# Performance work log

Hardware: AMD Instinct MI355X
Metric: run time of the kernel (lower is better)

The kernel has to match this reference:

```python
import jax, jax.numpy as jnp
import numpy as np

N = 100000
E = 1600000
IN_DIM = 64
H_DIM = 64
OUT_DIM = 1


def gcn_conv(x, edge_index, W, b):
    """PyG-style GCNConv: D^-1/2 (A + I) D^-1/2 X W + b."""
    n = x.shape[0]
    h = x @ W  # [N, h]
    src, dst = edge_index[0], edge_index[1]
    # degree with self-loops
    deg = jax.ops.segment_sum(jnp.ones(src.shape[0], x.dtype), dst, num_segments=n) + 1.0
    dinv = jax.lax.rsqrt(deg)  # deg >= 1 always (self-loops)
    # neighbor messages, symmetric normalization
    coef = dinv[src] * dinv[dst]                       # [E]
    msg = h[src] * coef[:, None]                       # [E, h]
    agg = jax.ops.segment_sum(msg, dst, num_segments=n)
    # self-loop contribution
    agg = agg + h * (dinv * dinv)[:, None]
    return agg + b


def setup_inputs() -> dict:
    key = jax.random.key(0)
    ks = jax.random.split(key, 14)
    s = lambda d: 1.0 / np.sqrt(d)
    return {
        "x": jax.random.normal(ks[0], (N, IN_DIM), jnp.float32),
        "edge_index": jax.random.randint(ks[1], (2, E), 0, N, jnp.int64),
        "fake_x": jax.random.normal(ks[2], (N, IN_DIM), jnp.float32),
        "fake_edge_index": jax.random.randint(ks[3], (2, E), 0, N, jnp.int64),
        "W1": jax.random.uniform(ks[4], (IN_DIM, H_DIM), jnp.float32, -s(IN_DIM), s(IN_DIM)),
        "b1": jnp.zeros((H_DIM,), jnp.float32),
        "W2": jax.random.uniform(ks[5], (H_DIM, H_DIM), jnp.float32, -s(H_DIM), s(H_DIM)),
        "b2": jnp.zeros((H_DIM,), jnp.float32),
        "Wy": jax.random.uniform(ks[6], (H_DIM, OUT_DIM), jnp.float32, -s(H_DIM), s(H_DIM)),
        "by": jnp.zeros((OUT_DIM,), jnp.float32),
        "Wp": jax.random.uniform(ks[7], (H_DIM, OUT_DIM), jnp.float32, -s(H_DIM), s(H_DIM)),
        "bp": jnp.zeros((OUT_DIM,), jnp.float32),
        "Wb": jax.random.uniform(ks[8], (H_DIM, OUT_DIM), jnp.float32, -s(H_DIM), s(H_DIM)),
        "bb": jnp.zeros((OUT_DIM,), jnp.float32),
    }


def reference(x, edge_index, fake_x, fake_edge_index,
              W1, b1, W2, b2, Wy, by, Wp, bp, Wb, bb):
    # eval mode: dropout is identity
    xZ1 = jax.nn.relu(gcn_conv(x, edge_index, W1, b1))
    xfZ1 = jax.nn.relu(gcn_conv(fake_x, fake_edge_index, W1, b1))
    xZ2 = gcn_conv(xZ1, edge_index, W2, b2)
    xfZ2 = gcn_conv(xfZ1, fake_edge_index, W2, b2)
    yi = jax.nn.relu(xZ2 @ Wy + by)
    fprob = jax.nn.relu(xZ2 @ Wp + bp)
    fprob_f = jax.nn.relu(xfZ2 @ Wp + bp)
    treat_prob = jax.nn.relu(xZ2 @ Wb + bb)
    return (yi, fprob, fprob_f, treat_prob)
```

## Files before the change

kernel.cpp:

```cpp
#include <hip/hip_runtime.h>
#include <hip/hip_bf16.h>

typedef __hip_bfloat16 bf16;

__device__ __forceinline__ float b2f(bf16 v) { return __bfloat162float(v); }
__device__ __forceinline__ float bu2f(unsigned short u) { return __uint_as_float(((unsigned)u) << 16); }
__device__ __forceinline__ unsigned short f2bu(float f) {
    bf16 h = __float2bfloat16(f);
    return *(unsigned short*)&h;
}

__device__ __forceinline__ int getIdx(const void* p, long long i, int is64) {
    return is64 ? (int)(((const long long*)p)[i]) : ((const int*)p)[i];
}
__device__ __forceinline__ float loadF(const void* p, size_t i, int isF32) {
    return isF32 ? ((const float*)p)[i] : b2f(((const bf16*)p)[i]);
}
__device__ __forceinline__ void storeF(void* p, size_t i, float v, int isF32) {
    if (isF32) ((float*)p)[i] = v;
    else       ((bf16*)p)[i]  = __float2bfloat16(v);
}

#define NPART 128
#define CHUNK 2048
#define BINCAP 40
#define MAXSLICE 800

__global__ void setup_kernel(const void* __restrict__ edge, const void* __restrict__ x,
                             const void* __restrict__ b2,
                             const void* __restrict__ Wy, const void* __restrict__ by,
                             const void* __restrict__ Wp, const void* __restrict__ bp,
                             const void* __restrict__ Wb, const void* __restrict__ bb,
                             float* __restrict__ c, int* __restrict__ flags,
                             int* __restrict__ bCntAll) {
    __shared__ int sh_isF32;
    const int tid  = threadIdx.x;
    const int lane = tid & 63;
    const int wv   = tid >> 6;
    bCntAll[tid] = 0;
    if (wv == 0) {
        const int* e32 = (const int*)edge;
        int nz = 0;
        for (int k = 1 + 2 * lane; k < 1024; k += 128) nz |= (e32[k] != 0);
        int allzero = !__any(nz);
        if (allzero) {
            int nz2 = 0;
            for (int k = 1000001 + 2 * lane; k < 1002048; k += 128) nz2 |= (e32[k] != 0);
            allzero = !__any(nz2);
        }
        const unsigned short* u = (const unsigned short*)x;
        int insane = 0;
        for (int k = 2 * lane; k < 512; k += 128) {
            int ex = (u[k] >> 7) & 0xFF;
            if (ex != 0 && (ex < 90 || ex > 160)) insane++;
        }
#pragma unroll
        for (int off = 32; off > 0; off >>= 1) insane += __shfl_xor(insane, off, 64);
        if (lane == 0) {
            flags[0] = allzero;
            flags[1] = (insane > 64) ? 1 : 0;
            sh_isF32 = (insane > 64) ? 1 : 0;
        }
    }
    __syncthreads();
    if (wv == 0) {
        const int isF32 = sh_isF32;
        float b = loadF(b2, lane, isF32);
        float cy = b * loadF(Wy, lane, isF32);
        float cp = b * loadF(Wp, lane, isF32);
        float cb = b * loadF(Wb, lane, isF32);
#pragma unroll
        for (int off = 32; off > 0; off >>= 1) {
            cy += __shfl_xor(cy, off, 64);
            cp += __shfl_xor(cp, off, 64);
            cb += __shfl_xor(cb, off, 64);
        }
        if (lane == 0) {
            c[0] = cy + loadF(by, 0, isF32);
            c[1] = cp + loadF(bp, 0, isF32);
            c[2] = cb + loadF(bb, 0, isF32);
        }
    }
}

__global__ void bucket_kernel(const void* __restrict__ e0, const void* __restrict__ e1,
                              int E, int N,
                              unsigned* __restrict__ bk0, unsigned* __restrict__ bk1,
                              int bucketCap, int* __restrict__ bCntBase,
                              const int* __restrict__ flags) {
    __shared__ unsigned bins[NPART][BINCAP];
    __shared__ int binCnt[NPART];
    __shared__ int binBase[NPART];
    const int g = blockIdx.y;
    const void* edge = g ? e1 : e0;
    unsigned* __restrict__ bucket = g ? bk1 : bk0;
    int* __restrict__ bCnt = bCntBase + g * NPART;
    const int is64 = flags[0];
    const int tid = threadIdx.x;
    long long base = (long long)blockIdx.x * CHUNK;
    if (base >= E) return;
    if (tid < NPART) binCnt[tid] = 0;
    __syncthreads();
    for (int k = tid; k < CHUNK; k += 256) {
        long long e = base + k;
        if (e < E) {
            int s = getIdx(edge, e, is64);
            int d = getIdx(edge, (long long)E + e, is64);
            int p = (int)(((long long)d * NPART) / N);
            if (p > NPART - 1) p = NPART - 1;
            int lo = (int)(((long long)N * p + NPART - 1) / NPART);
            unsigned packed = ((unsigned)s << 10) | (unsigned)(d - lo);
            int idx = atomicAdd(&binCnt[p], 1);
            if (idx < BINCAP) bins[p][idx] = packed;
            else {
                int pos = atomicAdd(&bCnt[p], 1);
                bucket[(size_t)p * bucketCap + pos] = packed;
            }
        }
    }
    __syncthreads();
    if (tid < NPART) {
        int cnt = min(binCnt[tid], BINCAP);
        binBase[tid] = atomicAdd(&bCnt[tid], cnt);
        binCnt[tid]  = cnt;
    }
    __syncthreads();
    for (int p = 0; p < NPART; ++p) {
        int cnt = binCnt[p];
        int gb  = binBase[p];
        unsigned* dstp = bucket + (size_t)p * bucketCap + gb;
        for (int k = tid; k < cnt; k += 256) dstp[k] = bins[p][k];
    }
}

__global__ void csr_build_kernel(const unsigned* __restrict__ bk0, const unsigned* __restrict__ bk1,
                                 int bucketCap, const int* __restrict__ bCntBase,
                                 int* __restrict__ rp0, int* __restrict__ rp1,
                                 float* __restrict__ dv0, float* __restrict__ dv1,
                                 int* __restrict__ cs0, int* __restrict__ cs1,
                                 int N, int E) {
    __shared__ int hist[MAXSLICE];
    __shared__ int tmp[1024];
    __shared__ int partBase;
    const int g = blockIdx.y;
    const unsigned* __restrict__ bucket = g ? bk1 : bk0;
    const int* __restrict__ bCnt = bCntBase + g * NPART;
    int*   __restrict__ rowptr  = g ? rp1 : rp0;
    float* __restrict__ dinv    = g ? dv1 : dv0;
    int*   __restrict__ csr_src = g ? cs1 : cs0;
    const int tid = threadIdx.x;
    const int p  = blockIdx.x;
    const int lo = (int)(((long long)N * p + NPART - 1) / NPART);
    const int hi = (int)(((long long)N * (p + 1) + NPART - 1) / NPART);
    const int nloc = hi - lo;
    const int cnt = bCnt[p];
    for (int t = tid; t < nloc; t += 1024) hist[t] = 0;
    if (tid == 0) {
        int b = 0;
        for (int q = 0; q < p; ++q) b += bCnt[q];
        partBase = b;
    }
    __syncthreads();
    const unsigned* __restrict__ seg = bucket + (size_t)p * bucketCap;
    for (int e = tid; e < cnt; e += 1024) atomicAdd(&hist[seg[e] & 1023u], 1);
    __syncthreads();
    const int k0 = tid * 2;
    const int s0 = (k0     < nloc) ? hist[k0]     : 0;
    const int s1 = (k0 + 1 < nloc) ? hist[k0 + 1] : 0;
    tmp[tid] = s0 + s1;
    __syncthreads();
#pragma unroll
    for (int off = 1; off < 1024; off <<= 1) {
        int v = (tid >= off) ? tmp[tid - off] : 0;
        __syncthreads();
        tmp[tid] += v;
        __syncthreads();
    }
    const int r0 = partBase + tmp[tid] - (s0 + s1);
    if (k0 < nloc) {
        rowptr[lo + k0] = r0;
        dinv[lo + k0]   = rsqrtf((float)s0 + 1.0f);
        hist[k0] = r0;
    }
    if (k0 + 1 < nloc) {
        rowptr[lo + k0 + 1] = r0 + s0;
        dinv[lo + k0 + 1]   = rsqrtf((float)s1 + 1.0f);
        hist[k0 + 1] = r0 + s0;
    }
    if (p == NPART - 1 && tid == 0) rowptr[N] = E;
    __syncthreads();
    int e = tid;
    for (; e + 3 * 1024 < cnt; e += 4 * 1024) {
        unsigned v0 = seg[e];
        unsigned v1 = seg[e + 1024];
        unsigned v2 = seg[e + 2048];
        unsigned v3 = seg[e + 3072];
        csr_src[atomicAdd(&hist[v0 & 1023u], 1)] = (int)(v0 >> 10);
        csr_src[atomicAdd(&hist[v1 & 1023u], 1)] = (int)(v1 >> 10);
        csr_src[atomicAdd(&hist[v2 & 1023u], 1)] = (int)(v2 >> 10);
        csr_src[atomicAdd(&hist[v3 & 1023u], 1)] = (int)(v3 >> 10);
    }
    for (; e < cnt; e += 1024) {
        unsigned v = seg[e];
        csr_src[atomicAdd(&hist[v & 1023u], 1)] = (int)(v >> 10);
    }
}

#define XSTR 68

__global__ void gemm64_kernel(const void* __restrict__ in0, const void* __restrict__ in1,
                              const void* __restrict__ W,
                              const float* __restrict__ dv0, const float* __restrict__ dv1,
                              unsigned short* __restrict__ o0, unsigned short* __restrict__ o1,
                              int N, const int* __restrict__ flags) {
    __shared__ float Wl[64 * 64];
    __shared__ float Xl[64 * XSTR];
    const int g = blockIdx.y;
    const void* __restrict__ in = g ? in1 : in0;
    const float* __restrict__ dinv = g ? dv1 : dv0;
    unsigned short* __restrict__ out = g ? o1 : o0;
    const int isF32 = flags[1];
    const int tid = threadIdx.x;
    if (isF32) {
        const float4* W4 = (const float4*)W;
        float4* Wl4 = (float4*)Wl;
        for (int t = tid; t < 64 * 16; t += 256) Wl4[t] = W4[t];
    } else {
        for (int t = tid; t < 64 * 64; t += 256) Wl[t] = b2f(((const bf16*)W)[t]);
    }
    const int lane = tid & 63;
    const int wave = tid >> 6;
    const int slot = lane >> 4;
    const int fi   = lane & 15;
    const int r0   = wave * 16 + slot;

    for (int base = blockIdx.x * 64; base < N; base += gridDim.x * 64) {
        __syncthreads();
        if (isF32) {
            const float4* in4 = (const float4*)in;
            for (int t = tid; t < 64 * 16; t += 256) {
                int r = t >> 4, c4 = t & 15;
                int gr = base + r;
                float4 v = (gr < N) ? in4[(size_t)gr * 16 + c4] : make_float4(0.f, 0.f, 0.f, 0.f);
                *(float4*)&Xl[r * XSTR + c4 * 4] = v;
            }
        } else {
            for (int t = tid; t < 64 * 64; t += 256) {
                int r = t >> 6, c = t & 63;
                int gr = base + r;
                Xl[r * XSTR + c] = (gr < N) ? b2f(((const bf16*)in)[(size_t)gr * 64 + c]) : 0.f;
            }
        }
        __syncthreads();

        float4 a0 = make_float4(0.f,0.f,0.f,0.f), a1 = a0, a2 = a0, a3 = a0;
#pragma unroll 2
        for (int k = 0; k < 64; k += 4) {
            float4 w0 = *(const float4*)&Wl[(k + 0) * 64 + fi * 4];
            float4 w1 = *(const float4*)&Wl[(k + 1) * 64 + fi * 4];
            float4 w2 = *(const float4*)&Wl[(k + 2) * 64 + fi * 4];
            float4 w3 = *(const float4*)&Wl[(k + 3) * 64 + fi * 4];
            float4 x0 = *(const float4*)&Xl[(r0 +  0) * XSTR + k];
            float4 x1 = *(const float4*)&Xl[(r0 +  4) * XSTR + k];
            float4 x2 = *(const float4*)&Xl[(r0 +  8) * XSTR + k];
            float4 x3 = *(const float4*)&Xl[(r0 + 12) * XSTR + k];
            a0.x=fmaf(x0.x,w0.x,a0.x); a0.y=fmaf(x0.x,w0.y,a0.y); a0.z=fmaf(x0.x,w0.z,a0.z); a0.w=fmaf(x0.x,w0.w,a0.w);
            a0.x=fmaf(x0.y,w1.x,a0.x); a0.y=fmaf(x0.y,w1.y,a0.y); a0.z=fmaf(x0.y,w1.z,a0.z); a0.w=fmaf(x0.y,w1.w,a0.w);
            a0.x=fmaf(x0.z,w2.x,a0.x); a0.y=fmaf(x0.z,w2.y,a0.y); a0.z=fmaf(x0.z,w2.z,a0.z); a0.w=fmaf(x0.z,w2.w,a0.w);
            a0.x=fmaf(x0.w,w3.x,a0.x); a0.y=fmaf(x0.w,w3.y,a0.y); a0.z=fmaf(x0.w,w3.z,a0.z); a0.w=fmaf(x0.w,w3.w,a0.w);
            a1.x=fmaf(x1.x,w0.x,a1.x); a1.y=fmaf(x1.x,w0.y,a1.y); a1.z=fmaf(x1.x,w0.z,a1.z); a1.w=fmaf(x1.x,w0.w,a1.w);
            a1.x=fmaf(x1.y,w1.x,a1.x); a1.y=fmaf(x1.y,w1.y,a1.y); a1.z=fmaf(x1.y,w1.z,a1.z); a1.w=fmaf(x1.y,w1.w,a1.w);
            a1.x=fmaf(x1.z,w2.x,a1.x); a1.y=fmaf(x1.z,w2.y,a1.y); a1.z=fmaf(x1.z,w2.z,a1.z); a1.w=fmaf(x1.z,w2.w,a1.w);
            a1.x=fmaf(x1.w,w3.x,a1.x); a1.y=fmaf(x1.w,w3.y,a1.y); a1.z=fmaf(x1.w,w3.z,a1.z); a1.w=fmaf(x1.w,w3.w,a1.w);
            a2.x=fmaf(x2.x,w0.x,a2.x); a2.y=fmaf(x2.x,w0.y,a2.y); a2.z=fmaf(x2.x,w0.z,a2.z); a2.w=fmaf(x2.x,w0.w,a2.w);
            a2.x=fmaf(x2.y,w1.x,a2.x); a2.y=fmaf(x2.y,w1.y,a2.y); a2.z=fmaf(x2.y,w1.z,a2.z); a2.w=fmaf(x2.y,w1.w,a2.w);
            a2.x=fmaf(x2.z,w2.x,a2.x); a2.y=fmaf(x2.z,w2.y,a2.y); a2.z=fmaf(x2.z,w2.z,a2.z); a2.w=fmaf(x2.z,w2.w,a2.w);
            a2.x=fmaf(x2.w,w3.x,a2.x); a2.y=fmaf(x2.w,w3.y,a2.y); a2.z=fmaf(x2.w,w3.z,a2.z); a2.w=fmaf(x2.w,w3.w,a2.w);
            a3.x=fmaf(x3.x,w0.x,a3.x); a3.y=fmaf(x3.x,w0.y,a3.y); a3.z=fmaf(x3.x,w0.z,a3.z); a3.w=fmaf(x3.x,w0.w,a3.w);
            a3.x=fmaf(x3.y,w1.x,a3.x); a3.y=fmaf(x3.y,w1.y,a3.y); a3.z=fmaf(x3.y,w1.z,a3.z); a3.w=fmaf(x3.y,w1.w,a3.w);
            a3.x=fmaf(x3.z,w2.x,a3.x); a3.y=fmaf(x3.z,w2.y,a3.y); a3.z=fmaf(x3.z,w2.z,a3.z); a3.w=fmaf(x3.z,w2.w,a3.w);
            a3.x=fmaf(x3.w,w3.x,a3.x); a3.y=fmaf(x3.w,w3.y,a3.y); a3.z=fmaf(x3.w,w3.z,a3.z); a3.w=fmaf(x3.w,w3.w,a3.w);
        }
        float4 acc[4] = {a0, a1, a2, a3};
#pragma unroll
        for (int j = 0; j < 4; ++j) {
            int r = base + r0 + 4 * j;
            if (r < N) {
                float d = dinv[r];
                ushort4 o;
                o.x = f2bu(acc[j].x * d); o.y = f2bu(acc[j].y * d);
                o.z = f2bu(acc[j].z * d); o.w = f2bu(acc[j].w * d);
                ((ushort4*)out)[(size_t)r * 16 + fi] = o;
            }
        }
    }
}

__global__ void gemm64_heads_kernel(const float* __restrict__ in0, const float* __restrict__ in1,
                                    const void* __restrict__ W,
                                    const float* __restrict__ dv0, const float* __restrict__ dv1,
                                    const void* __restrict__ Wy, const void* __restrict__ Wp,
                                    const void* __restrict__ Wb,
                                    float4* __restrict__ t40, float4* __restrict__ t41,
                                    int N, const int* __restrict__ flags) {
    __shared__ float Wl[64 * 64];
    __shared__ float Xl[64 * XSTR];
    const int g = blockIdx.y;
    const float* __restrict__ in = g ? in1 : in0;
    const float* __restrict__ dinv = g ? dv1 : dv0;
    float4* __restrict__ t4 = g ? t41 : t40;
    const int isF32 = flags[1];
    const int tid = threadIdx.x;
    if (isF32) {
        const float4* W4 = (const float4*)W;
        float4* Wl4 = (float4*)Wl;
        for (int t = tid; t < 64 * 16; t += 256) Wl4[t] = W4[t];
    } else {
        for (int t = tid; t < 64 * 64; t += 256) Wl[t] = b2f(((const bf16*)W)[t]);
    }
    const int lane = tid & 63;
    const int wave = tid >> 6;
    const int slot = lane >> 4;
    const int fi   = lane & 15;
    const int r0   = wave * 16 + slot;
    float4 wy4 = make_float4(loadF(Wy, fi*4+0, isF32), loadF(Wy, fi*4+1, isF32),
                             loadF(Wy, fi*4+2, isF32), loadF(Wy, fi*4+3, isF32));
    float4 wp4 = make_float4(loadF(Wp, fi*4+0, isF32), loadF(Wp, fi*4+1, isF32),
                             loadF(Wp, fi*4+2, isF32), loadF(Wp, fi*4+3, isF32));
    float4 wb4 = make_float4(loadF(Wb, fi*4+0, isF32), loadF(Wb, fi*4+1, isF32),
                             loadF(Wb, fi*4+2, isF32), loadF(Wb, fi*4+3, isF32));

    for (int base = blockIdx.x * 64; base < N; base += gridDim.x * 64) {
        __syncthreads();
        const float4* in4 = (const float4*)in;
        for (int t = tid; t < 64 * 16; t += 256) {
            int r = t >> 4, c4 = t & 15;
            int gr = base + r;
            float4 v = (gr < N) ? in4[(size_t)gr * 16 + c4] : make_float4(0.f, 0.f, 0.f, 0.f);
            v.x = fmaxf(v.x, 0.f); v.y = fmaxf(v.y, 0.f);
            v.z = fmaxf(v.z, 0.f); v.w = fmaxf(v.w, 0.f);
            *(float4*)&Xl[r * XSTR + c4 * 4] = v;
        }
        __syncthreads();

        float4 a0 = make_float4(0.f,0.f,0.f,0.f), a1 = a0, a2 = a0, a3 = a0;
#pragma unroll 2
        for (int k = 0; k < 64; k += 4) {
            float4 w0 = *(const float4*)&Wl[(k + 0) * 64 + fi * 4];
            float4 w1 = *(const float4*)&Wl[(k + 1) * 64 + fi * 4];
            float4 w2 = *(const float4*)&Wl[(k + 2) * 64 + fi * 4];
            float4 w3 = *(const float4*)&Wl[(k + 3) * 64 + fi * 4];
            float4 x0 = *(const float4*)&Xl[(r0 +  0) * XSTR + k];
            float4 x1 = *(const float4*)&Xl[(r0 +  4) * XSTR + k];
            float4 x2 = *(const float4*)&Xl[(r0 +  8) * XSTR + k];
            float4 x3 = *(const float4*)&Xl[(r0 + 12) * XSTR + k];
            a0.x=fmaf(x0.x,w0.x,a0.x); a0.y=fmaf(x0.x,w0.y,a0.y); a0.z=fmaf(x0.x,w0.z,a0.z); a0.w=fmaf(x0.x,w0.w,a0.w);
            a0.x=fmaf(x0.y,w1.x,a0.x); a0.y=fmaf(x0.y,w1.y,a0.y); a0.z=fmaf(x0.y,w1.z,a0.z); a0.w=fmaf(x0.y,w1.w,a0.w);
            a0.x=fmaf(x0.z,w2.x,a0.x); a0.y=fmaf(x0.z,w2.y,a0.y); a0.z=fmaf(x0.z,w2.z,a0.z); a0.w=fmaf(x0.z,w2.w,a0.w);
            a0.x=fmaf(x0.w,w3.x,a0.x); a0.y=fmaf(x0.w,w3.y,a0.y); a0.z=fmaf(x0.w,w3.z,a0.z); a0.w=fmaf(x0.w,w3.w,a0.w);
            a1.x=fmaf(x1.x,w0.x,a1.x); a1.y=fmaf(x1.x,w0.y,a1.y); a1.z=fmaf(x1.x,w0.z,a1.z); a1.w=fmaf(x1.x,w0.w,a1.w);
            a1.x=fmaf(x1.y,w1.x,a1.x); a1.y=fmaf(x1.y,w1.y,a1.y); a1.z=fmaf(x1.y,w1.z,a1.z); a1.w=fmaf(x1.y,w1.w,a1.w);
            a1.x=fmaf(x1.z,w2.x,a1.x); a1.y=fmaf(x1.z,w2.y,a1.y); a1.z=fmaf(x1.z,w2.z,a1.z); a1.w=fmaf(x1.z,w2.w,a1.w);
            a1.x=fmaf(x1.w,w3.x,a1.x); a1.y=fmaf(x1.w,w3.y,a1.y); a1.z=fmaf(x1.w,w3.z,a1.z); a1.w=fmaf(x1.w,w3.w,a1.w);
            a2.x=fmaf(x2.x,w0.x,a2.x); a2.y=fmaf(x2.x,w0.y,a2.y); a2.z=fmaf(x2.x,w0.z,a2.z); a2.w=fmaf(x2.x,w0.w,a2.w);
            a2.x=fmaf(x2.y,w1.x,a2.x); a2.y=fmaf(x2.y,w1.y,a2.y); a2.z=fmaf(x2.y,w1.z,a2.z); a2.w=fmaf(x2.y,w1.w,a2.w);
            a2.x=fmaf(x2.z,w2.x,a2.x); a2.y=fmaf(x2.z,w2.y,a2.y); a2.z=fmaf(x2.z,w2.z,a2.z); a2.w=fmaf(x2.z,w2.w,a2.w);
            a2.x=fmaf(x2.w,w3.x,a2.x); a2.y=fmaf(x2.w,w3.y,a2.y); a2.z=fmaf(x2.w,w3.z,a2.z); a2.w=fmaf(x2.w,w3.w,a2.w);
            a3.x=fmaf(x3.x,w0.x,a3.x); a3.y=fmaf(x3.x,w0.y,a3.y); a3.z=fmaf(x3.x,w0.z,a3.z); a3.w=fmaf(x3.x,w0.w,a3.w);
            a3.x=fmaf(x3.y,w1.x,a3.x); a3.y=fmaf(x3.y,w1.y,a3.y); a3.z=fmaf(x3.y,w1.z,a3.z); a3.w=fmaf(x3.y,w1.w,a3.w);
            a3.x=fmaf(x3.z,w2.x,a3.x); a3.y=fmaf(x3.z,w2.y,a3.y); a3.z=fmaf(x3.z,w2.z,a3.z); a3.w=fmaf(x3.z,w2.w,a3.w);
            a3.x=fmaf(x3.w,w3.x,a3.x); a3.y=fmaf(x3.w,w3.y,a3.y); a3.z=fmaf(x3.w,w3.z,a3.z); a3.w=fmaf(x3.w,w3.w,a3.w);
        }
        float4 acc[4] = {a0, a1, a2, a3};
#pragma unroll
        for (int j = 0; j < 4; ++j) {
            int r = base + r0 + 4 * j;
            float d = (r < N) ? dinv[r] : 0.f;
            float ty = d * (acc[j].x * wy4.x + acc[j].y * wy4.y + acc[j].z * wy4.z + acc[j].w * wy4.w);
            float tp = d * (acc[j].x * wp4.x + acc[j].y * wp4.y + acc[j].z * wp4.z + acc[j].w * wp4.w);
            float tb = d * (acc[j].x * wb4.x + acc[j].y * wb4.y + acc[j].z * wb4.z + acc[j].w * wb4.w);
#pragma unroll
            for (int off = 1; off < 16; off <<= 1) {
                ty += __shfl_xor(ty, off, 64);
                tp += __shfl_xor(tp, off, 64);
                tb += __shfl_xor(tb, off, 64);
            }
            if (fi == 0 && r < N) t4[r] = make_float4(ty, tp, tb, 0.0f);
        }
    }
}

__global__ void gather_kernel(const int* __restrict__ cs0, const int* __restrict__ cs1,
                              const int* __restrict__ rp0, const int* __restrict__ rp1,
                              const float* __restrict__ dv0, const float* __restrict__ dv1,
                              const unsigned short* __restrict__ hp0, const unsigned short* __restrict__ hp1,
                              const void* __restrict__ bias,
                              float* __restrict__ out0, float* __restrict__ out1,
                              int N, const int* __restrict__ flags) {
    const int g = blockIdx.y;
    const int* __restrict__ csr_src = g ? cs1 : cs0;
    const int* __restrict__ rowptr  = g ? rp1 : rp0;
    const float* __restrict__ dinv  = g ? dv1 : dv0;
    const unsigned short* __restrict__ hp = g ? hp1 : hp0;
    float* __restrict__ out = g ? out1 : out0;
    const int isF32 = flags[1];
    const int lane = threadIdx.x & 63;
    const int slot = lane >> 4;
    const int fi   = lane & 15;
    int i = blockIdx.x * (blockDim.x >> 6) + (threadIdx.x >> 6);
    if (i >= N) return;
    const int beg = rowptr[i];
    const int end = rowptr[i + 1];
    const ushort4* __restrict__ h4 = (const ushort4*)hp;

    float4 a0 = make_float4(0.f, 0.f, 0.f, 0.f);
    float4 a1 = make_float4(0.f, 0.f, 0.f, 0.f);
    float4 a2 = make_float4(0.f, 0.f, 0.f, 0.f);
    float4 a3 = make_float4(0.f, 0.f, 0.f, 0.f);
    int e = beg + slot;
    for (; e + 12 < end; e += 16) {
        int s0 = csr_src[e];
        int s1 = csr_src[e + 4];
        int s2 = csr_src[e + 8];
        int s3 = csr_src[e + 12];
        ushort4 u0 = h4[(size_t)s0 * 16 + fi];
        ushort4 u1 = h4[(size_t)s1 * 16 + fi];
        ushort4 u2 = h4[(size_t)s2 * 16 + fi];
        ushort4 u3 = h4[(size_t)s3 * 16 + fi];
        a0.x += bu2f(u0.x); a0.y += bu2f(u0.y); a0.z += bu2f(u0.z); a0.w += bu2f(u0.w);
        a1.x += bu2f(u1.x); a1.y += bu2f(u1.y); a1.z += bu2f(u1.z); a1.w += bu2f(u1.w);
        a2.x += bu2f(u2.x); a2.y += bu2f(u2.y); a2.z += bu2f(u2.z); a2.w += bu2f(u2.w);
        a3.x += bu2f(u3.x); a3.y += bu2f(u3.y); a3.z += bu2f(u3.z); a3.w += bu2f(u3.w);
    }
    for (; e < end; e += 4) {
        int s = csr_src[e];
        ushort4 u = h4[(size_t)s * 16 + fi];
        a0.x += bu2f(u.x); a0.y += bu2f(u.y); a0.z += bu2f(u.z); a0.w += bu2f(u.w);
    }
    a0.x += a1.x + a2.x + a3.x; a0.y += a1.y + a2.y + a3.y;
    a0.z += a1.z + a2.z + a3.z; a0.w += a1.w + a2.w + a3.w;
    a0.x += __shfl_xor(a0.x, 16, 64); a0.y += __shfl_xor(a0.y, 16, 64);
    a0.z += __shfl_xor(a0.z, 16, 64); a0.w += __shfl_xor(a0.w, 16, 64);
    a0.x += __shfl_xor(a0.x, 32, 64); a0.y += __shfl_xor(a0.y, 32, 64);
    a0.z += __shfl_xor(a0.z, 32, 64); a0.w += __shfl_xor(a0.w, 32, 64);

    if (slot == 0) {
        const float di = dinv[i];
        ushort4 ui = h4[(size_t)i * 16 + fi];
        float4 r;
        r.x = fmaf(a0.x + bu2f(ui.x), di, loadF(bias, fi * 4 + 0, isF32));
        r.y = fmaf(a0.y + bu2f(ui.y), di, loadF(bias, fi * 4 + 1, isF32));
        r.z = fmaf(a0.z + bu2f(ui.z), di, loadF(bias, fi * 4 + 2, isF32));
        r.w = fmaf(a0.w + bu2f(ui.w), di, loadF(bias, fi * 4 + 3, isF32));
        ((float4*)out)[(size_t)i * 16 + fi] = r;
    }
}

__global__ void gather_scalar_kernel(const int* __restrict__ cs0, const int* __restrict__ cs1,
                                     const int* __restrict__ rp0, const int* __restrict__ rp1,
                                     const float* __restrict__ dv0, const float* __restrict__ dv1,
                                     const float4* __restrict__ t40, const float4* __restrict__ t41,
                                     const float* __restrict__ c, void* __restrict__ out,
                                     int N, int gbase, const int* __restrict__ flags) {
    const int g = blockIdx.y;
    const int* __restrict__ csr_src = g ? cs1 : cs0;
    const int* __restrict__ rowptr  = g ? rp1 : rp0;
    const float* __restrict__ dinv  = g ? dv1 : dv0;
    const float4* __restrict__ t4   = g ? t41 : t40;
    const int mode = gbase + g;
    int tid  = blockIdx.x * blockDim.x + threadIdx.x;
    int i    = tid >> 2;
    int slot = tid & 3;
    if (i >= N) return;
    const int beg = rowptr[i];
    const int end = rowptr[i + 1];
    float ax = 0.f, ay = 0.f, az = 0.f;
    for (int e = beg + slot; e < end; e += 4) {
        float4 t = t4[csr_src[e]];
        ax += t.x; ay += t.y; az += t.z;
    }
    ax += __shfl_xor(ax, 1, 64); ay += __shfl_xor(ay, 1, 64); az += __shfl_xor(az, 1, 64);
    ax += __shfl_xor(ax, 2, 64); ay += __shfl_xor(ay, 2, 64); az += __shfl_xor(az, 2, 64);
    if (slot == 0) {
        const int isF32 = flags[1];
        float4 ti = t4[i];
        float di  = dinv[i];
        if (mode == 0) {
            storeF(out, (size_t)i,         fmaxf(fmaf(di, ax + ti.x, c[0]), 0.0f), isF32);
            storeF(out, (size_t)N + i,     fmaxf(fmaf(di, ay + ti.y, c[1]), 0.0f), isF32);
            storeF(out, (size_t)3 * N + i, fmaxf(fmaf(di, az + ti.z, c[2]), 0.0f), isF32);
        } else {
            storeF(out, (size_t)2 * N + i, fmaxf(fmaf(di, ay + ti.y, c[1]), 0.0f), isF32);
        }
    }
}

extern "C" void kernel_launch(void* const* d_in, const int* in_sizes, int n_in,
                              void* d_out, int out_size, void* d_ws, size_t ws_size,
                              hipStream_t stream) {
    const void* x   = d_in[0];
    const void* ei  = d_in[1];
    const void* fx  = d_in[2];
    const void* fei = d_in[3];
    const void* W1  = d_in[4];
    const void* b1  = d_in[5];
    const void* W2  = d_in[6];
    const void* b2  = d_in[7];
    const void* Wy  = d_in[8];
    const void* by  = d_in[9];
    const void* Wp  = d_in[10];
    const void* bp  = d_in[11];
    const void* Wb  = d_in[12];
    const void* bb  = d_in[13];

    const int N = in_sizes[0] / 64;
    const int E = in_sizes[1] / 2;
    const int bucketCap = E / NPART + 2048;

    char* base = (char*)d_ws;
    int dup = 2;
    int *flags = nullptr, *bCnt = nullptr;
    int *rp[2], *cs[2];
    unsigned* bk[2];
    float* dv[2];
    float* cvals = nullptr;
    unsigned short* bA[2];
    float* bB[2];
    float4* t4[2];

    for (int attempt = 0; attempt < 2; ++attempt) {
        size_t off = 0;
        auto alloc = [&](size_t bytes) { size_t r = (off + 15) & ~(size_t)15; off = r + bytes; return r; };
        size_t o_flags = alloc(16 * 4);
        size_t o_bcnt  = alloc(2 * NPART * 4);
        size_t o_rp[2], o_cs[2], o_bk[2], o_dv[2], o_bA[2], o_bB[2], o_t4[2], o_cv;
        for (int g = 0; g < dup; ++g) o_rp[g] = alloc((size_t)(N + 1) * 4);
        for (int g = 0; g < dup; ++g) o_cs[g] = alloc((size_t)E * 4);
        for (int g = 0; g < dup; ++g) o_bk[g] = alloc((size_t)NPART * bucketCap * 4);
        for (int g = 0; g < dup; ++g) o_dv[g] = alloc((size_t)N * 4);
        o_cv = alloc(16 * 4);
        for (int g = 0; g < dup; ++g) o_bA[g] = alloc((size_t)N * 64 * 2);
        for (int g = 0; g < dup; ++g) o_bB[g] = alloc((size_t)N * 64 * 4);
        for (int g = 0; g < dup; ++g) o_t4[g] = alloc((size_t)N * 16);
        if (off > ws_size && dup == 2) { dup = 1; continue; }
        flags = (int*)(base + o_flags);
        bCnt  = (int*)(base + o_bcnt);
        cvals = (float*)(base + o_cv);
        for (int g = 0; g < 2; ++g) {
            int s = (g < dup) ? g : 0;
            rp[g] = (int*)(base + o_rp[s]);
            cs[g] = (int*)(base + o_cs[s]);
            bk[g] = (unsigned*)(base + o_bk[s]);
            dv[g] = (float*)(base + o_dv[s]);
            bA[g] = (unsigned short*)(base + o_bA[s]);
            bB[g] = (float*)(base + o_bB[s]);
            t4[g] = (float4*)(base + o_t4[s]);
        }
        break;
    }

    const int THREADS = 256;
    const int nChunks = (E + CHUNK - 1) / CHUNK;
    const int nTiles  = (N + 63) / 64;
    const int nScal   = (4 * N + THREADS - 1) / THREADS;

    setup_kernel<<<1, 256, 0, stream>>>(ei, x, b2, Wy, by, Wp, bp, Wb, bb, cvals, flags, bCnt);

    if (dup == 2) {
        bucket_kernel<<<dim3(nChunks, 2), THREADS, 0, stream>>>(
            ei, fei, E, N, bk[0], bk[1], bucketCap, bCnt, flags);
        csr_build_kernel<<<dim3(NPART, 2), 1024, 0, stream>>>(
            bk[0], bk[1], bucketCap, bCnt, rp[0], rp[1], dv[0], dv[1], cs[0], cs[1], N, E);
        gemm64_kernel<<<dim3(nTiles, 2), THREADS, 0, stream>>>(
            x, fx, W1, dv[0], dv[1], bA[0], bA[1], N, flags);
        gather_kernel<<<dim3((N + 3) / 4, 2), THREADS, 0, stream>>>(
            cs[0], cs[1], rp[0], rp[1], dv[0], dv[1], bA[0], bA[1], b1, bB[0], bB[1], N, flags);
        gemm64_heads_kernel<<<dim3(nTiles, 2), THREADS, 0, stream>>>(
            bB[0], bB[1], W2, dv[0], dv[1], Wy, Wp, Wb, t4[0], t4[1], N, flags);
        gather_scalar_kernel<<<dim3(nScal, 2), THREADS, 0, stream>>>(
            cs[0], cs[1], rp[0], rp[1], dv[0], dv[1], t4[0], t4[1], cvals, d_out, N, 0, flags);
    } else {
        for (int g = 0; g < 2; ++g) {
            const void* xg   = g ? fx : x;
            const void* edge = g ? fei : ei;
            int* bCntg = bCnt + g * NPART;
            bucket_kernel<<<dim3(nChunks, 1), THREADS, 0, stream>>>(
                edge, edge, E, N, bk[0], bk[0], bucketCap, bCntg, flags);
            csr_build_kernel<<<dim3(NPART, 1), 1024, 0, stream>>>(
                bk[0], bk[0], bucketCap, bCntg, rp[0], rp[0], dv[0], dv[0], cs[0], cs[0], N, E);
            gemm64_kernel<<<dim3(nTiles, 1), THREADS, 0, stream>>>(
                xg, xg, W1, dv[0], dv[0], bA[0], bA[0], N, flags);
            gather_kernel<<<dim3((N + 3) / 4, 1), THREADS, 0, stream>>>(
                cs[0], cs[0], rp[0], rp[0], dv[0], dv[0], bA[0], bA[0], b1, bB[0], bB[0], N, flags);
            gemm64_heads_kernel<<<dim3(nTiles, 1), THREADS, 0, stream>>>(
                bB[0], bB[0], W2, dv[0], dv[0], Wy, Wp, Wb, t4[0], t4[0], N, flags);
            gather_scalar_kernel<<<dim3(nScal, 1), THREADS, 0, stream>>>(
                cs[0], cs[0], rp[0], rp[0], dv[0], dv[0], t4[0], t4[0], cvals, d_out, N, g, flags);
        }
    }
}
```

Before: 402.2 us.

## Fuse layer-1 gather with W2 projection and output heads into one kernel

Merges the layer-1 neighbor aggregation with the second GEMM and the three head dot-products. Each wave aggregates a node, applies bias and ReLU, multiplies by W2 (held in LDS) using wave shuffles, then reduces onto the three heads. This removes the N×64 fp32 intermediate buffer and one kernel launch, and switches the gather to a grid-stride loop with a fixed grid. The cost is a per-node 64×64 matvec done through broadcast shuffles plus a full 64-lane reduction, which adds ALU and shuffle work inside the latency-bound gather.

After: 505.2 us. 25.6% more time.

```diff
diff --git a/kernel.cpp b/kernel.cpp
--- a/kernel.cpp
+++ b/kernel.cpp
@@ -296,163 +296,108 @@
     }
 }
 
-__global__ void gemm64_heads_kernel(const float* __restrict__ in0, const float* __restrict__ in1,
-                                    const void* __restrict__ W,
+__global__ void gather_fused_kernel(const int* __restrict__ cs0, const int* __restrict__ cs1,
+                                    const int* __restrict__ rp0, const int* __restrict__ rp1,
                                     const float* __restrict__ dv0, const float* __restrict__ dv1,
+                                    const unsigned short* __restrict__ hp0, const unsigned short* __restrict__ hp1,
+                                    const void* __restrict__ bias, const void* __restrict__ W2,
                                     const void* __restrict__ Wy, const void* __restrict__ Wp,
                                     const void* __restrict__ Wb,
                                     float4* __restrict__ t40, float4* __restrict__ t41,
                                     int N, const int* __restrict__ flags) {
-    __shared__ float Wl[64 * 64];
-    __shared__ float Xl[64 * XSTR];
-    const int g = blockIdx.y;
-    const float* __restrict__ in = g ? in1 : in0;
-    const float* __restrict__ dinv = g ? dv1 : dv0;
-    float4* __restrict__ t4 = g ? t41 : t40;
-    const int isF32 = flags[1];
-    const int tid = threadIdx.x;
-    if (isF32) {
-        const float4* W4 = (const float4*)W;
-        float4* Wl4 = (float4*)Wl;
-        for (int t = tid; t < 64 * 16; t += 256) Wl4[t] = W4[t];
-    } else {
-        for (int t = tid; t < 64 * 64; t += 256) Wl[t] = b2f(((const bf16*)W)[t]);
-    }
-    const int lane = tid & 63;
-    const int wave = tid >> 6;
-    const int slot = lane >> 4;
-    const int fi   = lane & 15;
-    const int r0   = wave * 16 + slot;
-    float4 wy4 = make_float4(loadF(Wy, fi*4+0, isF32), loadF(Wy, fi*4+1, isF32),
-                             loadF(Wy, fi*4+2, isF32), loadF(Wy, fi*4+3, isF32));
-    float4 wp4 = make_float4(loadF(Wp, fi*4+0, isF32), loadF(Wp, fi*4+1, isF32),
-                             loadF(Wp, fi*4+2, isF32), loadF(Wp, fi*4+3, isF32));
-    float4 wb4 = make_float4(loadF(Wb, fi*4+0, isF32), loadF(Wb, fi*4+1, isF32),
-                             loadF(Wb, fi*4+2, isF32), loadF(Wb, fi*4+3, isF32));
-
-    for (int base = blockIdx.x * 64; base < N; base += gridDim.x * 64) {
-        __syncthreads();
-        const float4* in4 = (const float4*)in;
-        for (int t = tid; t < 64 * 16; t += 256) {
-            int r = t >> 4, c4 = t & 15;
-            int gr = base + r;
-            float4 v = (gr < N) ? in4[(size_t)gr * 16 + c4] : make_float4(0.f, 0.f, 0.f, 0.f);
-            v.x = fmaxf(v.x, 0.f); v.y = fmaxf(v.y, 0.f);
-            v.z = fmaxf(v.z, 0.f); v.w = fmaxf(v.w, 0.f);
-            *(float4*)&Xl[r * XSTR + c4 * 4] = v;
-        }
-        __syncthreads();
-
-        float4 a0 = make_float4(0.f,0.f,0.f,0.f), a1 = a0, a2 = a0, a3 = a0;
-#pragma unroll 2
-        for (int k = 0; k < 64; k += 4) {
-            float4 w0 = *(const float4*)&Wl[(k + 0) * 64 + fi * 4];
-            float4 w1 = *(const float4*)&Wl[(k + 1) * 64 + fi * 4];
-            float4 w2 = *(const float4*)&Wl[(k + 2) * 64 + fi * 4];
-            float4 w3 = *(const float4*)&Wl[(k + 3) * 64 + fi * 4];
-            float4 x0 = *(const float4*)&Xl[(r0 +  0) * XSTR + k];
-            float4 x1 = *(const float4*)&Xl[(r0 +  4) * XSTR + k];
-            float4 x2 = *(const float4*)&Xl[(r0 +  8) * XSTR + k];
-            float4 x3 = *(const float4*)&Xl[(r0 + 12) * XSTR + k];
-            a0.x=fmaf(x0.x,w0.x,a0.x); a0.y=fmaf(x0.x,w0.y,a0.y); a0.z=fmaf(x0.x,w0.z,a0.z); a0.w=fmaf(x0.x,w0.w,a0.w);
-            a0.x=fmaf(x0.y,w1.x,a0.x); a0.y=fmaf(x0.y,w1.y,a0.y); a0.z=fmaf(x0.y,w1.z,a0.z); a0.w=fmaf(x0.y,w1.w,a0.w);
-            a0.x=fmaf(x0.z,w2.x,a0.x); a0.y=fmaf(x0.z,w2.y,a0.y); a0.z=fmaf(x0.z,w2.z,a0.z); a0.w=fmaf(x0.z,w2.w,a0.w);
-            a0.x=fmaf(x0.w,w3.x,a0.x); a0.y=fmaf(x0.w,w3.y,a0.y); a0.z=fmaf(x0.w,w3.z,a0.z); a0.w=fmaf(x0.w,w3.w,a0.w);
-            a1.x=fmaf(x1.x,w0.x,a1.x); a1.y=fmaf(x1.x,w0.y,a1.y); a1.z=fmaf(x1.x,w0.z,a1.z); a1.w=fmaf(x1.x,w0.w,a1.w);
-            a1.x=fmaf(x1.y,w1.x,a1.x); a1.y=fmaf(x1.y,w1.y,a1.y); a1.z=fmaf(x1.y,w1.z,a1.z); a1.w=fmaf(x1.y,w1.w,a1.w);
-            a1.x=fmaf(x1.z,w2.x,a1.x); a1.y=fmaf(x1.z,w2.y,a1.y); a1.z=fmaf(x1.z,w2.z,a1.z); a1.w=fmaf(x1.z,w2.w,a1.w);
-            a1.x=fmaf(x1.w,w3.x,a1.x); a1.y=fmaf(x1.w,w3.y,a1.y); a1.z=fmaf(x1.w,w3.z,a1.z); a1.w=fmaf(x1.w,w3.w,a1.w);
-            a2.x=fmaf(x2.x,w0.x,a2.x); a2.y=fmaf(x2.x,w0.y,a2.y); a2.z=fmaf(x2.x,w0.z,a2.z); a2.w=fmaf(x2.x,w0.w,a2.w);
-            a2.x=fmaf(x2.y,w1.x,a2.x); a2.y=fmaf(x2.y,w1.y,a2.y); a2.z=fmaf(x2.y,w1.z,a2.z); a2.w=fmaf(x2.y,w1.w,a2.w);
-            a2.x=fmaf(x2.z,w2.x,a2.x); a2.y=fmaf(x2.z,w2.y,a2.y); a2.z=fmaf(x2.z,w2.z,a2.z); a2.w=fmaf(x2.z,w2.w,a2.w);
-            a2.x=fmaf(x2.w,w3.x,a2.x); a2.y=fmaf(x2.w,w3.y,a2.y); a2.z=fmaf(x2.w,w3.z,a2.z); a2.w=fmaf(x2.w,w3.w,a2.w);
-            a3.x=fmaf(x3.x,w0.x,a3.x); a3.y=fmaf(x3.x,w0.y,a3.y); a3.z=fmaf(x3.x,w0.z,a3.z); a3.w=fmaf(x3.x,w0.w,a3.w);
-            a3.x=fmaf(x3.y,w1.x,a3.x); a3.y=fmaf(x3.y,w1.y,a3.y); a3.z=fmaf(x3.y,w1.z,a3.z); a3.w=fmaf(x3.y,w1.w,a3.w);
-            a3.x=fmaf(x3.z,w2.x,a3.x); a3.y=fmaf(x3.z,w2.y,a3.y); a3.z=fmaf(x3.z,w2.z,a3.z); a3.w=fmaf(x3.z,w2.w,a3.w);
-            a3.x=fmaf(x3.w,w3.x,a3.x); a3.y=fmaf(x3.w,w3.y,a3.y); a3.z=fmaf(x3.w,w3.z,a3.z); a3.w=fmaf(x3.w,w3.w,a3.w);
-        }
-        float4 acc[4] = {a0, a1, a2, a3};
-#pragma unroll
-        for (int j = 0; j < 4; ++j) {
-            int r = base + r0 + 4 * j;
-            float d = (r < N) ? dinv[r] : 0.f;
-            float ty = d * (acc[j].x * wy4.x + acc[j].y * wy4.y + acc[j].z * wy4.z + acc[j].w * wy4.w);
-            float tp = d * (acc[j].x * wp4.x + acc[j].y * wp4.y + acc[j].z * wp4.z + acc[j].w * wp4.w);
-            float tb = d * (acc[j].x * wb4.x + acc[j].y * wb4.y + acc[j].z * wb4.z + acc[j].w * wb4.w);
-#pragma unroll
-            for (int off = 1; off < 16; off <<= 1) {
-                ty += __shfl_xor(ty, off, 64);
-                tp += __shfl_xor(tp, off, 64);
-                tb += __shfl_xor(tb, off, 64);
-            }
-            if (fi == 0 && r < N) t4[r] = make_float4(ty, tp, tb, 0.0f);
-        }
-    }
-}
-
-__global__ void gather_kernel(const int* __restrict__ cs0, const int* __restrict__ cs1,
-                              const int* __restrict__ rp0, const int* __restrict__ rp1,
-                              const float* __restrict__ dv0, const float* __restrict__ dv1,
-                              const unsigned short* __restrict__ hp0, const unsigned short* __restrict__ hp1,
-                              const void* __restrict__ bias,
-                              float* __restrict__ out0, float* __restrict__ out1,
-                              int N, const int* __restrict__ flags) {
+    __shared__ float W2l[64 * 64];
     const int g = blockIdx.y;
     const int* __restrict__ csr_src = g ? cs1 : cs0;
     const int* __restrict__ rowptr  = g ? rp1 : rp0;
     const float* __restrict__ dinv  = g ? dv1 : dv0;
     const unsigned short* __restrict__ hp = g ? hp1 : hp0;
-    float* __restrict__ out = g ? out1 : out0;
+    float4* __restrict__ t4 = g ? t41 : t40;
     const int isF32 = flags[1];
-    const int lane = threadIdx.x & 63;
+    const int tid = threadIdx.x;
+    if (isF32) {
+        const float4* W4 = (const float4*)W2;
+        float4* Wl4 = (float4*)W2l;
+        for (int t = tid; t < 64 * 16; t += 256) Wl4[t] = W4[t];
+    } else {
+        for (int t = tid; t < 64 * 64; t += 256) W2l[t] = b2f(((const bf16*)W2)[t]);
+    }
+    __syncthreads();
+
+    const int lane = tid & 63;
     const int slot = lane >> 4;
     const int fi   = lane & 15;
-    int i = blockIdx.x * (blockDim.x >> 6) + (threadIdx.x >> 6);
-    if (i >= N) return;
-    const int beg = rowptr[i];
-    const int end = rowptr[i + 1];
+    const int wv   = tid >> 6;
     const ushort4* __restrict__ h4 = (const ushort4*)hp;
-
-    float4 a0 = make_float4(0.f, 0.f, 0.f, 0.f);
-    float4 a1 = make_float4(0.f, 0.f, 0.f, 0.f);
-    float4 a2 = make_float4(0.f, 0.f, 0.f, 0.f);
-    float4 a3 = make_float4(0.f, 0.f, 0.f, 0.f);
-    int e = beg + slot;
-    for (; e + 12 < end; e += 16) {
-        int s0 = csr_src[e];
-        int s1 = csr_src[e + 4];
-        int s2 = csr_src[e + 8];
-        int s3 = csr_src[e + 12];
-        ushort4 u0 = h4[(size_t)s0 * 16 + fi];
-        ushort4 u1 = h4[(size_t)s1 * 16 + fi];
-        ushort4 u2 = h4[(size_t)s2 * 16 + fi];
-        ushort4 u3 = h4[(size_t)s3 * 16 + fi];
-        a0.x += bu2f(u0.x); a0.y += bu2f(u0.y); a0.z += bu2f(u0.z); a0.w += bu2f(u0.w);
-        a1.x += bu2f(u1.x); a1.y += bu2f(u1.y); a1.z += bu2f(u1.z); a1.w += bu2f(u1.w);
-        a2.x += bu2f(u2.x); a2.y += bu2f(u2.y); a2.z += bu2f(u2.z); a2.w += bu2f(u2.w);
-        a3.x += bu2f(u3.x); a3.y += bu2f(u3.y); a3.z += bu2f(u3.z); a3.w += bu2f(u3.w);
-    }
-    for (; e < end; e += 4) {
-        int s = csr_src[e];
-        ushort4 u = h4[(size_t)s * 16 + fi];
-        a0.x += bu2f(u.x); a0.y += bu2f(u.y); a0.z += bu2f(u.z); a0.w += bu2f(u.w);
-    }
-    a0.x += a1.x + a2.x + a3.x; a0.y += a1.y + a2.y + a3.y;
-    a0.z += a1.z + a2.z + a3.z; a0.w += a1.w + a2.w + a3.w;
-    a0.x += __shfl_xor(a0.x, 16, 64); a0.y += __shfl_xor(a0.y, 16, 64);
-    a0.z += __shfl_xor(a0.z, 16, 64); a0.w += __shfl_xor(a0.w, 16, 64);
-    a0.x += __shfl_xor(a0.x, 32, 64); a0.y += __shfl_xor(a0.y, 32, 64);
-    a0.z += __shfl_xor(a0.z, 32, 64); a0.w += __shfl_xor(a0.w, 32, 64);
-
-    if (slot == 0) {
+    const float wyj = loadF(Wy, lane, isF32);
+    const float wpj = loadF(Wp, lane, isF32);
+    const float wbj = loadF(Wb, lane, isF32);
+    float4 bias4 = make_float4(loadF(bias, fi * 4 + 0, isF32), loadF(bias, fi * 4 + 1, isF32),
+                               loadF(bias, fi * 4 + 2, isF32), loadF(bias, fi * 4 + 3, isF32));
+
+    const int wavesAll = gridDim.x * (blockDim.x >> 6);
+    for (int i = blockIdx.x * (blockDim.x >> 6) + wv; i < N; i += wavesAll) {
+        const int beg = rowptr[i];
+        const int end = rowptr[i + 1];
+        float4 a0 = make_float4(0.f, 0.f, 0.f, 0.f);
+        float4 a1 = make_float4(0.f, 0.f, 0.f, 0.f);
+        float4 a2 = make_float4(0.f, 0.f, 0.f, 0.f);
+        float4 a3 = make_float4(0.f, 0.f, 0.f, 0.f);
+        int e = beg + slot;
+        for (; e + 12 < end; e += 16) {
+            int s0 = csr_src[e];
+            int s1 = csr_src[e + 4];
+            int s2 = csr_src[e + 8];
+            int s3 = csr_src[e + 12];
+            ushort4 u0 = h4[(size_t)s0 * 16 + fi];
+            ushort4 u1 = h4[(size_t)s1 * 16 + fi];
+            ushort4 u2 = h4[(size_t)s2 * 16 + fi];
+            ushort4 u3 = h4[(size_t)s3 * 16 + fi];
+            a0.x += bu2f(u0.x); a0.y += bu2f(u0.y); a0.z += bu2f(u0.z); a0.w += bu2f(u0.w);
+            a1.x += bu2f(u1.x); a1.y += bu2f(u1.y); a1.z += bu2f(u1.z); a1.w += bu2f(u1.w);
+            a2.x += bu2f(u2.x); a2.y += bu2f(u2.y); a2.z += bu2f(u2.z); a2.w += bu2f(u2.w);
+            a3.x += bu2f(u3.x); a3.y += bu2f(u3.y); a3.z += bu2f(u3.z); a3.w += bu2f(u3.w);
+        }
+        for (; e < end; e += 4) {
+            int s = csr_src[e];
+            ushort4 u = h4[(size_t)s * 16 + fi];
+            a0.x += bu2f(u.x); a0.y += bu2f(u.y); a0.z += bu2f(u.z); a0.w += bu2f(u.w);
+        }
+        a0.x += a1.x + a2.x + a3.x; a0.y += a1.y + a2.y + a3.y;
+        a0.z += a1.z + a2.z + a3.z; a0.w += a1.w + a2.w + a3.w;
+        a0.x += __shfl_xor(a0.x, 16, 64); a0.y += __shfl_xor(a0.y, 16, 64);
+        a0.z += __shfl_xor(a0.z, 16, 64); a0.w += __shfl_xor(a0.w, 16, 64);
+        a0.x += __shfl_xor(a0.x, 32, 64); a0.y += __shfl_xor(a0.y, 32, 64);
+        a0.z += __shfl_xor(a0.z, 32, 64); a0.w += __shfl_xor(a0.w, 32, 64);
+
         const float di = dinv[i];
         ushort4 ui = h4[(size_t)i * 16 + fi];
-        float4 r;
-        r.x = fmaf(a0.x + bu2f(ui.x), di, loadF(bias, fi * 4 + 0, isF32));
-        r.y = fmaf(a0.y + bu2f(ui.y), di, loadF(bias, fi * 4 + 1, isF32));
-        r.z = fmaf(a0.z + bu2f(ui.z), di, loadF(bias, fi * 4 + 2, isF32));
-        r.w = fmaf(a0.w + bu2f(ui.w), di, loadF(bias, fi * 4 + 3, isF32));
-        ((float4*)out)[(size_t)i * 16 + fi] = r;
+        float4 v;
+        v.x = fmaxf(fmaf(a0.x + bu2f(ui.x), di, bias4.x), 0.f);
+        v.y = fmaxf(fmaf(a0.y + bu2f(ui.y), di, bias4.y), 0.f);
+        v.z = fmaxf(fmaf(a0.z + bu2f(ui.z), di, bias4.z), 0.f);
+        v.w = fmaxf(fmaf(a0.w + bu2f(ui.w), di, bias4.w), 0.f);
+
+        float h2 = 0.f;
+#pragma unroll
+        for (int q = 0; q < 16; ++q) {
+            float bx = __shfl(v.x, q, 64);
+            float by = __shfl(v.y, q, 64);
+            float bz = __shfl(v.z, q, 64);
+            float bw = __shfl(v.w, q, 64);
+            h2 = fmaf(bx, W2l[(4 * q + 0) * 64 + lane], h2);
+            h2 = fmaf(by, W2l[(4 * q + 1) * 64 + lane], h2);
+            h2 = fmaf(bz, W2l[(4 * q + 2) * 64 + lane], h2);
+            h2 = fmaf(bw, W2l[(4 * q + 3) * 64 + lane], h2);
+        }
+        h2 *= di;
+        float ty = h2 * wyj, tp = h2 * wpj, tb = h2 * wbj;
+#pragma unroll
+        for (int off = 1; off < 64; off <<= 1) {
+            ty += __shfl_xor(ty, off, 64);
+            tp += __shfl_xor(tp, off, 64);
+            tb += __shfl_xor(tb, off, 64);
+        }
+        if (lane == 0) t4[i] = make_float4(ty, tp, tb, 0.0f);
     }
 }
 
@@ -525,7 +470,6 @@
     float* dv[2];
     float* cvals = nullptr;
     unsigned short* bA[2];
-    float* bB[2];
     float4* t4[2];
 
     for (int attempt = 0; attempt < 2; ++attempt) {
@@ -533,14 +477,13 @@
         auto alloc = [&](size_t bytes) { size_t r = (off + 15) & ~(size_t)15; off = r + bytes; return r; };
         size_t o_flags = alloc(16 * 4);
         size_t o_bcnt  = alloc(2 * NPART * 4);
-        size_t o_rp[2], o_cs[2], o_bk[2], o_dv[2], o_bA[2], o_bB[2], o_t4[2], o_cv;
+        size_t o_rp[2], o_cs[2], o_bk[2], o_dv[2], o_bA[2], o_t4[2], o_cv;
         for (int g = 0; g < dup; ++g) o_rp[g] = alloc((size_t)(N + 1) * 4);
         for (int g = 0; g < dup; ++g) o_cs[g] = alloc((size_t)E * 4);
         for (int g = 0; g < dup; ++g) o_bk[g] = alloc((size_t)NPART * bucketCap * 4);
         for (int g = 0; g < dup; ++g) o_dv[g] = alloc((size_t)N * 4);
         o_cv = alloc(16 * 4);
         for (int g = 0; g < dup; ++g) o_bA[g] = alloc((size_t)N * 64 * 2);
-        for (int g = 0; g < dup; ++g) o_bB[g] = alloc((size_t)N * 64 * 4);
         for (int g = 0; g < dup; ++g) o_t4[g] = alloc((size_t)N * 16);
         if (off > ws_size && dup == 2) { dup = 1; continue; }
         flags = (int*)(base + o_flags);
@@ -553,7 +496,6 @@
             bk[g] = (unsigned*)(base + o_bk[s]);
             dv[g] = (float*)(base + o_dv[s]);
             bA[g] = (unsigned short*)(base + o_bA[s]);
-            bB[g] = (float*)(base + o_bB[s]);
             t4[g] = (float4*)(base + o_t4[s]);
         }
         break;
@@ -563,6 +505,7 @@
     const int nChunks = (E + CHUNK - 1) / CHUNK;
     const int nTiles  = (N + 63) / 64;
     const int nScal   = (4 * N + THREADS - 1) / THREADS;
+    const int nGather = 1024;
 
     setup_kernel<<<1, 256, 0, stream>>>(ei, x, b2, Wy, by, Wp, bp, Wb, bb, cvals, flags, bCnt);
 
@@ -573,10 +516,9 @@
             bk[0], bk[1], bucketCap, bCnt, rp[0], rp[1], dv[0], dv[1], cs[0], cs[1], N, E);
         gemm64_kernel<<<dim3(nTiles, 2), THREADS, 0, stream>>>(
             x, fx, W1, dv[0], dv[1], bA[0], bA[1], N, flags);
-        gather_kernel<<<dim3((N + 3) / 4, 2), THREADS, 0, stream>>>(
-            cs[0], cs[1], rp[0], rp[1], dv[0], dv[1], bA[0], bA[1], b1, bB[0], bB[1], N, flags);
-        gemm64_heads_kernel<<<dim3(nTiles, 2), THREADS, 0, stream>>>(
-            bB[0], bB[1], W2, dv[0], dv[1], Wy, Wp, Wb, t4[0], t4[1], N, flags);
+        gather_fused_kernel<<<dim3(nGather, 2), THREADS, 0, stream>>>(
+            cs[0], cs[1], rp[0], rp[1], dv[0], dv[1], bA[0], bA[1], b1, W2,
+            Wy, Wp, Wb, t4[0], t4[1], N, flags);
         gather_scalar_kernel<<<dim3(nScal, 2), THREADS, 0, stream>>>(
             cs[0], cs[1], rp[0], rp[1], dv[0], dv[1], t4[0], t4[1], cvals, d_out, N, 0, flags);
     } else {
@@ -590,10 +532,9 @@
                 bk[0], bk[0], bucketCap, bCntg, rp[0], rp[0], dv[0], dv[0], cs[0], cs[0], N, E);
             gemm64_kernel<<<dim3(nTiles, 1), THREADS, 0, stream>>>(
                 xg, xg, W1, dv[0], dv[0], bA[0], bA[0], N, flags);
-            gather_kernel<<<dim3((N + 3) / 4, 1), THREADS, 0, stream>>>(
-                cs[0], cs[0], rp[0], rp[0], dv[0], dv[0], bA[0], bA[0], b1, bB[0], bB[0], N, flags);
-            gemm64_heads_kernel<<<dim3(nTiles, 1), THREADS, 0, stream>>>(
-                bB[0], bB[0], W2, dv[0], dv[0], Wy, Wp, Wb, t4[0], t4[0], N, flags);
+            gather_fused_kernel<<<dim3(nGather, 1), THREADS, 0, stream>>>(
+                cs[0], cs[0], rp[0], rp[0], dv[0], dv[0], bA[0], bA[0], b1, W2,
+                Wy, Wp, Wb, t4[0], t4[0], N, flags);
             gather_scalar_kernel<<<dim3(nScal, 1), THREADS, 0, stream>>>(
                 cs[0], cs[0], rp[0], rp[0], dv[0], dv[0], t4[0], t4[0], cvals, d_out, N, g, flags);
         }
```
